# Kernel tuning notes

Hardware: AMD Instinct MI355X
Metric: run time of the kernel (lower is better)

Reference implementation:

```python
import jax, jax.numpy as jnp
import numpy as np

B, S, D, L = 64, 4096, 256, 16

def setup_inputs() -> dict:
    key = jax.random.key(0)
    k1, k2, k3 = jax.random.split(key, 3)
    right_emb = jax.random.normal(k1, (B, S, D), dtype=jnp.float32)
    # pair_id in [-1, L): -1 means identity passthrough (as in the torch forward)
    pair_id = jax.random.randint(k2, (B, 1), -1, L, dtype=jnp.int32)
    # kaiming-uniform-ish random mapping matrices (reset_with_identity=False)
    mapping = jax.random.normal(k3, (L, D, D), dtype=jnp.float32) * (1.0 / np.sqrt(D))
    return {"right_emb": right_emb, "mapping": mapping, "pair_id": pair_id}

def reference(right_emb, mapping, pair_id):
    # lang id per sample; -1 -> passthrough
    lang = pair_id[:, 0]                      # [B]
    passthrough = lang < 0                    # [B] bool
    Wg = mapping[jnp.clip(lang, 0)]           # [B, D, D] gathered per-sample matrices
    # F.linear(x, W) == x @ W^T : out[b,s,e] = sum_d x[b,s,d] * W[b,e,d]
    out = jnp.einsum('bsd,bed->bse', right_emb, Wg)
    return jnp.where(passthrough[:, None, None], right_emb, out)
```

## Files before the change

### kernel.cpp

```cpp
#include <hip/hip_runtime.h>


typedef __attribute__((ext_vector_type(8))) short bf16x8;
typedef __attribute__((ext_vector_type(16))) float f32x16;

#define S_DIM 4096
#define D_DIM 256
#define BM 64
#define BK 64
#define NT 256

static __device__ __forceinline__ unsigned short f2bf(float f) {
    unsigned int u = __float_as_uint(f);
    return (unsigned short)((u + 0x7fffu + ((u >> 16) & 1u)) >> 16);
}

static __device__ __forceinline__ unsigned int pack_bf2(float lo, float hi) {
    unsigned int a = __float_as_uint(lo), b = __float_as_uint(hi);
    a += 0x7fffu + ((a >> 16) & 1u);
    b += 0x7fffu + ((b >> 16) & 1u);
    return (a >> 16) | (b & 0xffff0000u);
}

static __device__ __forceinline__ void dma16(const void* g, void* l) {
    __builtin_amdgcn_global_load_lds(
        (const __attribute__((address_space(1))) unsigned int*)g,
        (__attribute__((address_space(3))) unsigned int*)l, 16, 0, 0);
}

__global__ void cvt_w_kernel(const float* __restrict__ w, unsigned short* __restrict__ wb) {
    int i = (blockIdx.x * 256 + threadIdx.x) * 4;
    float4 v = *(const float4*)(w + i);
    ushort4 p;
    p.x = f2bf(v.x); p.y = f2bf(v.y); p.z = f2bf(v.z); p.w = f2bf(v.w);
    *(ushort4*)(wb + i) = p;
}

__global__ __launch_bounds__(NT, 3) void MultipleMappings_5952824672291_kernel(
    const float* __restrict__ X, const unsigned short* __restrict__ Wb,
    const int* __restrict__ pair_id, float* __restrict__ Y)
{
    __shared__ unsigned short ldsW[256 * 64];
    __shared__ float ldsA[64 * 64];

    const int b = blockIdx.y;
    const int t = threadIdx.x;
    const long base = ((long)b * S_DIM + (long)blockIdx.x * BM) * D_DIM;
    const float* Xb = X + base;
    float* Yb = Y + base;
    const int lang = pair_id[b];

    if (lang < 0) {
        #pragma unroll
        for (int i = 0; i < 16; ++i) {
            int f4 = t + i * NT;
            *(float4*)(Yb + (long)f4 * 4) = *(const float4*)(Xb + (long)f4 * 4);
        }
        return;
    }

    const unsigned short* Wl = Wb + (size_t)lang * (D_DIM * D_DIM);

    const int lane  = t & 63;
    const int wave  = t >> 6;
    const int wr    = wave >> 1;
    const int wc    = wave & 1;
    const int lrow  = lane & 31;
    const int khalf = lane >> 5;

    f32x16 acc[4] = {};

    for (int kc = 0; kc < 4; ++kc) {
        __syncthreads();
        #pragma unroll
        for (int j = 0; j < 8; ++j) {
            int slot = j * NT + t;
            int row = slot >> 3, kgl = slot & 7;
            int kgs = kgl ^ (row & 7);
            dma16(Wl + row * D_DIM + kc * BK + kgs * 8, (char*)ldsW + slot * 16);
        }
        #pragma unroll
        for (int j = 0; j < 4; ++j) {
            int slot = j * NT + t;
            int row = slot >> 4, kgl = slot & 15;
            int kgs = kgl ^ (row & 15);
            dma16(Xb + row * D_DIM + kc * BK + kgs * 4, (char*)ldsA + slot * 16);
        }
        __syncthreads();
        #pragma unroll
        for (int kk = 0; kk < 4; ++kk) {
            const int k = kk * 16 + khalf * 8;
            const int arow = wr * 32 + lrow;
            const int am = arow & 15;
            const int kg0 = k >> 2;
            float4 a0 = *(const float4*)((char*)ldsA + arow * 256 + ((kg0 ^ am) * 16));
            float4 a1 = *(const float4*)((char*)ldsA + arow * 256 + (((kg0 + 1) ^ am) * 16));
            union { bf16x8 v; unsigned int u[4]; } af;
            af.u[0] = pack_bf2(a0.x, a0.y);
            af.u[1] = pack_bf2(a0.z, a0.w);
            af.u[2] = pack_bf2(a1.x, a1.y);
            af.u[3] = pack_bf2(a1.z, a1.w);
            const int kg = k >> 3;
            #pragma unroll
            for (int ct = 0; ct < 4; ++ct) {
                const int brow = wc * 128 + ct * 32 + lrow;
                bf16x8 bfv = *(const bf16x8*)((char*)ldsW + brow * 128 + ((kg ^ (brow & 7)) * 16));
                acc[ct] = __builtin_amdgcn_mfma_f32_32x32x16_bf16(af.v, bfv, acc[ct], 0, 0, 0);
            }
        }
    }

    #pragma unroll
    for (int ct = 0; ct < 4; ++ct) {
        const int colg = wc * 128 + ct * 32 + lrow;
        #pragma unroll
        for (int r = 0; r < 16; ++r) {
            int rowg = wr * 32 + 4 * khalf + (r & 3) + 8 * (r >> 2);
            Yb[(long)rowg * D_DIM + colg] = acc[ct][r];
        }
    }
}

extern "C" void kernel_launch(void* const* d_in, const int* in_sizes, int n_in,
                              void* d_out, int out_size, void* d_ws, size_t ws_size,
                              hipStream_t stream) {
    const float* X   = (const float*)d_in[0];
    const float* W   = (const float*)d_in[1];
    const int*   pid = (const int*)d_in[2];
    float*       Y   = (float*)d_out;
    unsigned short* Wbf = (unsigned short*)d_ws;

    cvt_w_kernel<<<dim3(1024), dim3(256), 0, stream>>>(W, Wbf);

    dim3 grid(S_DIM / BM, 64);
    MultipleMappings_5952824672291_kernel<<<grid, dim3(NT), 0, stream>>>(X, Wbf, pid, Y);
}
```

Measured before the change: 441.1 us.

## Pre-swizzle weights into MFMA fragment layout and drop LDS staging

```diff
diff --git a/kernel.cpp b/kernel.cpp
--- a/kernel.cpp
+++ b/kernel.cpp
@@ -3,17 +3,11 @@
 
 typedef __attribute__((ext_vector_type(8))) short bf16x8;
 typedef __attribute__((ext_vector_type(16))) float f32x16;
+typedef __attribute__((ext_vector_type(4))) float f32x4;
 
 #define S_DIM 4096
 #define D_DIM 256
-#define BM 64
-#define BK 64
 #define NT 256
-
-static __device__ __forceinline__ unsigned short f2bf(float f) {
-    unsigned int u = __float_as_uint(f);
-    return (unsigned short)((u + 0x7fffu + ((u >> 16) & 1u)) >> 16);
-}
 
 static __device__ __forceinline__ unsigned int pack_bf2(float lo, float hi) {
     unsigned int a = __float_as_uint(lo), b = __float_as_uint(hi);
@@ -22,102 +16,78 @@
     return (a >> 16) | (b & 0xffff0000u);
 }
 
-static __device__ __forceinline__ void dma16(const void* g, void* l) {
-    __builtin_amdgcn_global_load_lds(
-        (const __attribute__((address_space(1))) unsigned int*)g,
-        (__attribute__((address_space(3))) unsigned int*)l, 16, 0, 0);
+__global__ void cvt_w_kernel(const float* __restrict__ w, unsigned short* __restrict__ wb) {
+    int t = blockIdx.x * NT + threadIdx.x;
+    int lane = t & 63;
+    int k16  = (t >> 6) & 15;
+    int cg   = (t >> 10) & 7;
+    int lang = t >> 13;
+    int lrow = lane & 31, khalf = lane >> 5;
+    const float* src = w + (((size_t)(lang << 8) + (cg << 5) + lrow) << 8) + (k16 << 4) + (khalf << 3);
+    f32x4 v0 = *(const f32x4*)src;
+    f32x4 v1 = *(const f32x4*)(src + 4);
+    union { bf16x8 v; unsigned int u[4]; } p;
+    p.u[0] = pack_bf2(v0.x, v0.y);
+    p.u[1] = pack_bf2(v0.z, v0.w);
+    p.u[2] = pack_bf2(v1.x, v1.y);
+    p.u[3] = pack_bf2(v1.z, v1.w);
+    *(bf16x8*)(wb + (size_t)t * 8) = p.v;
 }
 
-__global__ void cvt_w_kernel(const float* __restrict__ w, unsigned short* __restrict__ wb) {
-    int i = (blockIdx.x * 256 + threadIdx.x) * 4;
-    float4 v = *(const float4*)(w + i);
-    ushort4 p;
-    p.x = f2bf(v.x); p.y = f2bf(v.y); p.z = f2bf(v.z); p.w = f2bf(v.w);
-    *(ushort4*)(wb + i) = p;
-}
-
-__global__ __launch_bounds__(NT, 3) void MultipleMappings_5952824672291_kernel(
+__global__ __launch_bounds__(NT, 4) void MultipleMappings_5952824672291_kernel(
     const float* __restrict__ X, const unsigned short* __restrict__ Wb,
     const int* __restrict__ pair_id, float* __restrict__ Y)
 {
-    __shared__ unsigned short ldsW[256 * 64];
-    __shared__ float ldsA[64 * 64];
-
     const int b = blockIdx.y;
-    const int t = threadIdx.x;
-    const long base = ((long)b * S_DIM + (long)blockIdx.x * BM) * D_DIM;
+    const long base = ((long)b * S_DIM + (long)blockIdx.x * 32) * D_DIM;
     const float* Xb = X + base;
     float* Yb = Y + base;
     const int lang = pair_id[b];
+    const int t = threadIdx.x;
 
     if (lang < 0) {
         #pragma unroll
-        for (int i = 0; i < 16; ++i) {
+        for (int i = 0; i < 8; ++i) {
             int f4 = t + i * NT;
-            *(float4*)(Yb + (long)f4 * 4) = *(const float4*)(Xb + (long)f4 * 4);
+            f32x4 v = *(const f32x4*)(Xb + (long)f4 * 4);
+            __builtin_nontemporal_store(v, (f32x4*)(Yb + (long)f4 * 4));
         }
         return;
     }
 
-    const unsigned short* Wl = Wb + (size_t)lang * (D_DIM * D_DIM);
-
     const int lane  = t & 63;
     const int wave  = t >> 6;
-    const int wr    = wave >> 1;
-    const int wc    = wave & 1;
     const int lrow  = lane & 31;
     const int khalf = lane >> 5;
 
-    f32x16 acc[4] = {};
+    const float* xrow = Xb + (long)lrow * D_DIM + khalf * 8;
+    const unsigned short* wl  = Wb + (size_t)lang * (8 * 16 * 64 * 8);
+    const unsigned short* wt0 = wl + (size_t)(wave * 2 + 0) * (16 * 512) + lane * 8;
+    const unsigned short* wt1 = wl + (size_t)(wave * 2 + 1) * (16 * 512) + lane * 8;
 
-    for (int kc = 0; kc < 4; ++kc) {
-        __syncthreads();
-        #pragma unroll
-        for (int j = 0; j < 8; ++j) {
-            int slot = j * NT + t;
-            int row = slot >> 3, kgl = slot & 7;
-            int kgs = kgl ^ (row & 7);
-            dma16(Wl + row * D_DIM + kc * BK + kgs * 8, (char*)ldsW + slot * 16);
-        }
-        #pragma unroll
-        for (int j = 0; j < 4; ++j) {
-            int slot = j * NT + t;
-            int row = slot >> 4, kgl = slot & 15;
-            int kgs = kgl ^ (row & 15);
-            dma16(Xb + row * D_DIM + kc * BK + kgs * 4, (char*)ldsA + slot * 16);
-        }
-        __syncthreads();
-        #pragma unroll
-        for (int kk = 0; kk < 4; ++kk) {
-            const int k = kk * 16 + khalf * 8;
-            const int arow = wr * 32 + lrow;
-            const int am = arow & 15;
-            const int kg0 = k >> 2;
-            float4 a0 = *(const float4*)((char*)ldsA + arow * 256 + ((kg0 ^ am) * 16));
-            float4 a1 = *(const float4*)((char*)ldsA + arow * 256 + (((kg0 + 1) ^ am) * 16));
-            union { bf16x8 v; unsigned int u[4]; } af;
-            af.u[0] = pack_bf2(a0.x, a0.y);
-            af.u[1] = pack_bf2(a0.z, a0.w);
-            af.u[2] = pack_bf2(a1.x, a1.y);
-            af.u[3] = pack_bf2(a1.z, a1.w);
-            const int kg = k >> 3;
-            #pragma unroll
-            for (int ct = 0; ct < 4; ++ct) {
-                const int brow = wc * 128 + ct * 32 + lrow;
-                bf16x8 bfv = *(const bf16x8*)((char*)ldsW + brow * 128 + ((kg ^ (brow & 7)) * 16));
-                acc[ct] = __builtin_amdgcn_mfma_f32_32x32x16_bf16(af.v, bfv, acc[ct], 0, 0, 0);
-            }
-        }
+    f32x16 acc0 = {}, acc1 = {};
+
+    #pragma unroll 4
+    for (int k16 = 0; k16 < 16; ++k16) {
+        f32x4 a0 = *(const f32x4*)(xrow + k16 * 16);
+        f32x4 a1 = *(const f32x4*)(xrow + k16 * 16 + 4);
+        union { bf16x8 v; unsigned int u[4]; } af;
+        af.u[0] = pack_bf2(a0.x, a0.y);
+        af.u[1] = pack_bf2(a0.z, a0.w);
+        af.u[2] = pack_bf2(a1.x, a1.y);
+        af.u[3] = pack_bf2(a1.z, a1.w);
+        bf16x8 b0 = *(const bf16x8*)(wt0 + (size_t)k16 * 512);
+        bf16x8 b1 = *(const bf16x8*)(wt1 + (size_t)k16 * 512);
+        acc0 = __builtin_amdgcn_mfma_f32_32x32x16_bf16(af.v, b0, acc0, 0, 0, 0);
+        acc1 = __builtin_amdgcn_mfma_f32_32x32x16_bf16(af.v, b1, acc1, 0, 0, 0);
     }
 
     #pragma unroll
-    for (int ct = 0; ct < 4; ++ct) {
-        const int colg = wc * 128 + ct * 32 + lrow;
-        #pragma unroll
-        for (int r = 0; r < 16; ++r) {
-            int rowg = wr * 32 + 4 * khalf + (r & 3) + 8 * (r >> 2);
-            Yb[(long)rowg * D_DIM + colg] = acc[ct][r];
-        }
+    for (int r = 0; r < 16; ++r) {
+        int rowg = 4 * khalf + (r & 3) + 8 * (r >> 2);
+        float* yr = Yb + (long)rowg * D_DIM + wave * 64 + lrow;
+        __builtin_nontemporal_store(acc0[r], yr);
+        __builtin_nontemporal_store(acc1[r], yr + 32);
     }
 }
 
@@ -130,8 +100,8 @@
     float*       Y   = (float*)d_out;
     unsigned short* Wbf = (unsigned short*)d_ws;
 
-    cvt_w_kernel<<<dim3(1024), dim3(256), 0, stream>>>(W, Wbf);
+    cvt_w_kernel<<<dim3(512), dim3(NT), 0, stream>>>(W, Wbf);
 
-    dim3 grid(S_DIM / BM, 64);
+    dim3 grid(S_DIM / 32, 64);
     MultipleMappings_5952824672291_kernel<<<grid, dim3(NT), 0, stream>>>(X, Wbf, pid, Y);
 }
```

After: 566.2 us. 1.28x slower.
